# Kernel tuning notes

Hardware: AMD Instinct MI355X
Metric: run time of the kernel (lower is better)

The kernel has to match this reference:

```python
import jax, jax.numpy as jnp
import numpy as np

# Static hyperparameters (match init_kwargs)
PAD = 4          # one_side_pad_length
KL = 9           # kernel_size (= 2*PAD + 1 so L_out == output_size with stride 1)
STRIDE = 1
NLC = 8          # num_sparse_LC
OUT = 4096       # output_size


def _repeat_lengths():
    padded = OUT + 2 * PAD                      # 4104
    rough = padded // NLC                       # 513
    lens = []
    total = 0
    for i in range(NLC):
        if i == NLC - 1:
            cover = OUT - total
        else:
            cover = rough - 2 * PAD
        lens.append(cover)
        total += cover
    return lens                                  # [505]*7 + [561]


def setup_inputs() -> dict:
    key = jax.random.key(0)
    k1, k2, k3 = jax.random.split(key, 3)
    x = jax.random.normal(k1, (8, 2, 4, 64, 4096), dtype=jnp.float32)
    # weight: (dim_d, dim_k, out, in, num_sparse_LC, 1, kernel_size)
    weight = jax.random.normal(k2, (2, 4, 64, 64, 8, 1, 9), dtype=jnp.float32) * 0.05
    # conv_bias_param: (dim_d, dim_k, out, num_sparse_LC, 1)
    conv_bias_param = jax.random.normal(k3, (2, 4, 64, 8, 1), dtype=jnp.float32) * 0.02
    return {"x": x, "weight": weight, "conv_bias_param": conv_bias_param}


def reference(x, weight, conv_bias_param):
    # x: (b, d, k, in, L)
    x_pad = jnp.pad(x, ((0, 0), (0, 0), (0, 0), (0, 0), (PAD, PAD)))
    # unfold(-1, KL, 1): x_unf[..., l, f] = x_pad[..., l + f]; shape (b,d,k,in,OUT,KL)
    x_unf = jnp.stack([x_pad[..., f:f + OUT] for f in range(KL)], axis=-1)
    lens = _repeat_lengths()
    outs = []
    start = 0
    for i in range(NLC):  # small fixed loop over segments (avoids repeated-weight materialization)
        ln = lens[i]
        w = weight[:, :, :, :, i, 0, :]                 # (d, k, o, in, kl)
        xs = x_unf[:, :, :, :, start:start + ln, :]     # (b, d, k, in, ln, kl)
        o = jnp.einsum('dkoif,bdkilf->bdkol', w, xs)    # (b, d, k, o, ln)
        o = o + conv_bias_param[None, :, :, :, i, :]    # bias broadcasts over b and l
        outs.append(o)
        start += ln
    return jnp.concatenate(outs, axis=-1)               # (b, d, k, o, OUT)
```

## Files before the change

kernel.cpp:

```cpp
#include <hip/hip_runtime.h>

typedef __attribute__((ext_vector_type(8))) short bf16x8;
typedef __attribute__((ext_vector_type(4))) float f32x4;

#define WT2_BYTES (8ull * 8 * 9 * 8192)

#define AS1C(p) ((const __attribute__((address_space(1))) void*)(p))
#define AS3(p)  ((__attribute__((address_space(3))) void*)(p))

static __device__ __forceinline__ ushort f2bf(float f) {
    union { float f; unsigned u; } v; v.f = f;
    unsigned r = v.u + 0x7FFF + ((v.u >> 16) & 1);
    return (ushort)(r >> 16);
}
static __device__ __forceinline__ unsigned cvtpk(float a, float b) {
    unsigned r;
    asm("v_cvt_pk_bf16_f32 %0, %1, %2" : "=v"(r) : "v"(a), "v"(b));
    return r;
}

__global__ __launch_bounds__(256) void wprep3_kernel(const float* __restrict__ w,
                                                     ushort* __restrict__ wt) {
    __shared__ float raw[4608];
    __shared__ ushort row[72 * 64];
    int bid = blockIdx.x;
    int dk = bid >> 6, o = bid & 63;
    const float* src = w + (size_t)bid * 4608;
    int t = threadIdx.x;
    #pragma unroll
    for (int j = 0; j < 18; ++j) raw[t + 256 * j] = src[t + 256 * j];
    __syncthreads();
    int osw = o & 7;
    #pragma unroll
    for (int p = 0; p < 18; ++p) {
        int idx = t + 256 * p;
        int cf = idx >> 6, i = idx & 63;
        int c = cf / 9, f = cf - c * 9;
        row[cf * 64 + ((i >> 3) ^ osw) * 8 + (i & 7)] = f2bf(raw[i * 72 + c * 9 + f]);
    }
    __syncthreads();
    char* wb = (char*)wt + (size_t)dk * 8 * 9 * 8192 + o * 128;
    #pragma unroll
    for (int q = 0; q < 3; ++q) {
        int idx = q * 256 + t;
        if (idx < 576) {
            int cf = idx >> 3, cc = idx & 7;
            *(uint4*)(wb + (size_t)cf * 8192 + cc * 16) = *(const uint4*)&row[cf * 64 + cc * 8];
        }
    }
}

__global__ __launch_bounds__(256, 3) void conv10_kernel(
    const float* __restrict__ x, const ushort* __restrict__ wt,
    const float* __restrict__ bias, float* __restrict__ out)
{
    __shared__ __align__(16) ushort XL[136 * 64];
    __shared__ __align__(16) ushort WL[4 * 4096];

    int bid = blockIdx.x;
    int bdk = bid / 33, tile = bid - bdk * 33;
    int dk = bdk & 7;
    int c, lt;
    if (tile < 28) { c = tile >> 2; lt = tile & 3; } else { c = 7; lt = tile - 28; }
    int Sc = 505 * c, lb = lt << 7;
    int V = ((c == 7) ? 561 : 505) - lb; if (V > 128) V = 128;
    int R0 = Sc + lb;

    int t = threadIdx.x, lane = t & 63, wv = t >> 6;
    int ln16 = lane & 15, g = lane >> 4;
    int wr = wv >> 1, wc = wv & 1;
    int Lw = wr << 6, Ow = wc << 5;

    int lq = t & 31, ig = t >> 5;
    const float* xb = x + (size_t)bdk * 64 * 4096;
    float4 v[8];
    bool edge = (R0 < 4) || (R0 > 3972);
    if (!edge) {
        const float* xp = xb + (size_t)ig * 8 * 4096 + (R0 - 4 + lq * 4);
        #pragma unroll
        for (int j = 0; j < 8; ++j)
            v[j] = *(const float4*)(xp + (size_t)j * 4096);
    } else {
        #pragma unroll
        for (int j = 0; j < 8; ++j) {
            float* pv = (float*)&v[j];
            #pragma unroll
            for (int k = 0; k < 4; ++k) {
                int xr = R0 - 4 + lq * 4 + k;
                bool ok = (xr >= 0) && (xr < 4096);
                int xc = ok ? xr : 0;
                pv[k] = ok ? xb[(size_t)(ig * 8 + j) * 4096 + xc] : 0.0f;
            }
        }
    }
    float hv[8]; int rh = 0, igh = 0; bool okh = false;
    if (t < 64) {
        rh = 128 + (t >> 3);
        igh = t & 7;
        int xr = R0 - 4 + rh;
        okh = xr < 4096;
        int xc = okh ? xr : 0;
        const float* xh = xb + (size_t)igh * 8 * 4096 + xc;
        #pragma unroll
        for (int j = 0; j < 8; ++j) hv[j] = okh ? xh[(size_t)j * 4096] : 0.0f;
    }

    const char* wsl = (const char*)wt + (size_t)(dk * 8 + c) * 9 * 8192;
    auto stageW = [&](int f, int buf) {
        __builtin_amdgcn_global_load_lds(AS1C(wsl + (size_t)f * 8192 + t * 16),
                                         AS3((char*)WL + buf * 8192 + t * 16), 16, 0, 0);
        __builtin_amdgcn_global_load_lds(AS1C(wsl + (size_t)f * 8192 + 4096 + t * 16),
                                         AS3((char*)WL + buf * 8192 + 4096 + t * 16), 16, 0, 0);
    };
    stageW(0, 0); stageW(1, 1); stageW(2, 2);

    #pragma unroll
    for (int k = 0; k < 4; ++k) {
        int r = lq * 4 + k;
        uint4 A;
        A.x = cvtpk(((const float*)&v[0])[k], ((const float*)&v[1])[k]);
        A.y = cvtpk(((const float*)&v[2])[k], ((const float*)&v[3])[k]);
        A.z = cvtpk(((const float*)&v[4])[k], ((const float*)&v[5])[k]);
        A.w = cvtpk(((const float*)&v[6])[k], ((const float*)&v[7])[k]);
        *(uint4*)((char*)XL + r * 128 + ((ig ^ (r & 7)) * 16)) = A;
    }
    if (t < 64) {
        uint4 A;
        A.x = cvtpk(hv[0], hv[1]); A.y = cvtpk(hv[2], hv[3]);
        A.z = cvtpk(hv[4], hv[5]); A.w = cvtpk(hv[6], hv[7]);
        *(uint4*)((char*)XL + rh * 128 + ((igh ^ (rh & 7)) * 16)) = A;
    }

    f32x4 acc[4][2];
    #pragma unroll
    for (int a0 = 0; a0 < 4; ++a0)
        #pragma unroll
        for (int a1 = 0; a1 < 2; ++a1) acc[a0][a1] = (f32x4){0.f, 0.f, 0.f, 0.f};

    auto tap = [&](int f) {
        int buf = f & 3;
        int rbase = Lw + ln16 + f;
        int swz = rbase & 7;
        #pragma unroll
        for (int s = 0; s < 2; ++s) {
            int cof = ((s * 4 + g) ^ swz) * 16;
            int wof = buf * 8192 + ((s * 4 + g) ^ (ln16 & 7)) * 16;
            bf16x8 av[4], bv[2];
            #pragma unroll
            for (int mf = 0; mf < 4; ++mf)
                av[mf] = *(const bf16x8*)((const char*)XL + (rbase + mf * 16) * 128 + cof);
            #pragma unroll
            for (int nf = 0; nf < 2; ++nf)
                bv[nf] = *(const bf16x8*)((const char*)WL + wof + (Ow + nf * 16 + ln16) * 128);
            #pragma unroll
            for (int mf = 0; mf < 4; ++mf)
                #pragma unroll
                for (int nf = 0; nf < 2; ++nf)
                    acc[mf][nf] = __builtin_amdgcn_mfma_f32_16x16x32_bf16(av[mf], bv[nf], acc[mf][nf], 0, 0, 0);
        }
    };

    asm volatile("s_waitcnt lgkmcnt(0)" ::: "memory");

#define TAPSTEP(N, F, ISSUE) \
    asm volatile("s_waitcnt vmcnt(" #N ")" ::: "memory"); \
    __builtin_amdgcn_s_barrier(); \
    __builtin_amdgcn_sched_barrier(0); \
    if (ISSUE) stageW(F + 3, (F + 3) & 3); \
    tap(F);

    TAPSTEP(4, 0, 1) TAPSTEP(4, 1, 1) TAPSTEP(4, 2, 1) TAPSTEP(4, 3, 1)
    TAPSTEP(4, 4, 1) TAPSTEP(4, 5, 1) TAPSTEP(4, 6, 0) TAPSTEP(2, 7, 0)
    TAPSTEP(0, 8, 0)
#undef TAPSTEP

    float* ob = out + ((size_t)(bdk * 64)) * 4096 + Sc + lb;
    #pragma unroll
    for (int nf = 0; nf < 2; ++nf) {
        int o = Ow + nf * 16 + ln16;
        float bvs = bias[(dk * 64 + o) * 8 + c];
        #pragma unroll
        for (int mf = 0; mf < 4; ++mf) {
            int l = Lw + mf * 16 + g * 4;
            f32x4 vv = acc[mf][nf];
            vv[0] += bvs; vv[1] += bvs; vv[2] += bvs; vv[3] += bvs;
            if (l + 4 <= V) {
                *(f32x4*)(ob + (size_t)o * 4096 + l) = vv;
            } else if (l < V) {
                #pragma unroll
                for (int r = 0; r < 4; ++r)
                    if (l + r < V) ob[(size_t)o * 4096 + l + r] = vv[r];
            }
        }
    }
}

extern "C" void kernel_launch(void* const* d_in, const int* in_sizes, int n_in,
                              void* d_out, int out_size, void* d_ws, size_t ws_size,
                              hipStream_t stream) {
    const float* x    = (const float*)d_in[0];
    const float* wgt  = (const float*)d_in[1];
    const float* bias = (const float*)d_in[2];
    float* out        = (float*)d_out;
    ushort* wt2       = (ushort*)d_ws;

    hipLaunchKernelGGL(wprep3_kernel, dim3(512), dim3(256), 0, stream, wgt, wt2);
    hipLaunchKernelGGL(conv10_kernel, dim3(2112), dim3(256), 0, stream, x, wt2, bias, out);
}
```

Measured before the change: 55.63 us.

## Make conv kernel persistent and prefetch next tile's input during taps

Converts the one-tile-per-block conv kernel into a persistent kernel with 768 blocks striding over the 2112 tiles. The next tile's x slice is loaded into registers midway through the current tile's tap loop and written to LDS after the epilogue. This aims to hide global-load latency for x and remove per-block launch overhead and tail effects. In exchange it raises register pressure, which could hurt occupancy at 3 blocks per CU. The fixed 768-block grid may also leave an uneven tail, since 2112 tiles is not a multiple of 768.

```diff
diff --git a/kernel.cpp b/kernel.cpp
--- a/kernel.cpp
+++ b/kernel.cpp
@@ -50,93 +50,89 @@
     }
 }
 
-__global__ __launch_bounds__(256, 3) void conv10_kernel(
+__global__ __launch_bounds__(256, 3) void conv17_kernel(
     const float* __restrict__ x, const ushort* __restrict__ wt,
     const float* __restrict__ bias, float* __restrict__ out)
 {
     __shared__ __align__(16) ushort XL[136 * 64];
     __shared__ __align__(16) ushort WL[4 * 4096];
 
-    int bid = blockIdx.x;
-    int bdk = bid / 33, tile = bid - bdk * 33;
-    int dk = bdk & 7;
-    int c, lt;
-    if (tile < 28) { c = tile >> 2; lt = tile & 3; } else { c = 7; lt = tile - 28; }
-    int Sc = 505 * c, lb = lt << 7;
-    int V = ((c == 7) ? 561 : 505) - lb; if (V > 128) V = 128;
-    int R0 = Sc + lb;
-
+    const int NT = 2112, GS = 768;
     int t = threadIdx.x, lane = t & 63, wv = t >> 6;
     int ln16 = lane & 15, g = lane >> 4;
     int wr = wv >> 1, wc = wv & 1;
     int Lw = wr << 6, Ow = wc << 5;
-
     int lq = t & 31, ig = t >> 5;
-    const float* xb = x + (size_t)bdk * 64 * 4096;
-    float4 v[8];
-    bool edge = (R0 < 4) || (R0 > 3972);
-    if (!edge) {
-        const float* xp = xb + (size_t)ig * 8 * 4096 + (R0 - 4 + lq * 4);
-        #pragma unroll
-        for (int j = 0; j < 8; ++j)
-            v[j] = *(const float4*)(xp + (size_t)j * 4096);
-    } else {
-        #pragma unroll
-        for (int j = 0; j < 8; ++j) {
-            float* pv = (float*)&v[j];
-            #pragma unroll
-            for (int k = 0; k < 4; ++k) {
-                int xr = R0 - 4 + lq * 4 + k;
-                bool ok = (xr >= 0) && (xr < 4096);
-                int xc = ok ? xr : 0;
-                pv[k] = ok ? xb[(size_t)(ig * 8 + j) * 4096 + xc] : 0.0f;
+    int rh = 128 + (lane >> 3), igh = lane & 7;
+
+    auto dec = [&](int tid, int& bdk, int& dk, int& c, int& V, int& R0) {
+        bdk = tid / 33; int tile = tid - bdk * 33;
+        dk = bdk & 7;
+        int lt;
+        if (tile < 28) { c = tile >> 2; lt = tile & 3; } else { c = 7; lt = tile - 28; }
+        int lb = lt << 7;
+        V = ((c == 7) ? 561 : 505) - lb; if (V > 128) V = 128;
+        R0 = 505 * c + lb;
+    };
+
+    float4 v[8]; float hv[8];
+    auto xload = [&](int bdkX, int R0X) {
+        const float* xb = x + (size_t)bdkX * 64 * 4096;
+        bool edge = (R0X < 4) || (R0X > 3964);
+        if (!edge) {
+            const float* xp = xb + (size_t)ig * 8 * 4096 + (R0X - 4 + lq * 4);
+            #pragma unroll
+            for (int j = 0; j < 8; ++j)
+                v[j] = *(const float4*)(xp + (size_t)j * 4096);
+        } else {
+            #pragma unroll
+            for (int j = 0; j < 8; ++j) {
+                float* pv = (float*)&v[j];
+                #pragma unroll
+                for (int k = 0; k < 4; ++k) {
+                    int xr = R0X - 4 + lq * 4 + k;
+                    bool ok = (xr >= 0) && (xr < 4096);
+                    int xc = ok ? xr : 0;
+                    pv[k] = ok ? xb[(size_t)(ig * 8 + j) * 4096 + xc] : 0.0f;
+                }
             }
         }
-    }
-    float hv[8]; int rh = 0, igh = 0; bool okh = false;
-    if (t < 64) {
-        rh = 128 + (t >> 3);
-        igh = t & 7;
-        int xr = R0 - 4 + rh;
-        okh = xr < 4096;
-        int xc = okh ? xr : 0;
-        const float* xh = xb + (size_t)igh * 8 * 4096 + xc;
-        #pragma unroll
-        for (int j = 0; j < 8; ++j) hv[j] = okh ? xh[(size_t)j * 4096] : 0.0f;
-    }
-
-    const char* wsl = (const char*)wt + (size_t)(dk * 8 + c) * 9 * 8192;
-    auto stageW = [&](int f, int buf) {
+        {
+            int xr = R0X - 4 + rh;
+            bool okh = xr < 4096;
+            int xc = okh ? xr : 0;
+            const float* xh = xb + (size_t)igh * 8 * 4096 + xc;
+            #pragma unroll
+            for (int j = 0; j < 8; ++j) hv[j] = okh ? xh[(size_t)j * 4096] : 0.0f;
+        }
+    };
+    auto xwrite = [&]() {
+        #pragma unroll
+        for (int k = 0; k < 4; ++k) {
+            int r = lq * 4 + k;
+            uint4 A;
+            A.x = cvtpk(((const float*)&v[0])[k], ((const float*)&v[1])[k]);
+            A.y = cvtpk(((const float*)&v[2])[k], ((const float*)&v[3])[k]);
+            A.z = cvtpk(((const float*)&v[4])[k], ((const float*)&v[5])[k]);
+            A.w = cvtpk(((const float*)&v[6])[k], ((const float*)&v[7])[k]);
+            *(uint4*)((char*)XL + r * 128 + ((ig ^ (r & 7)) * 16)) = A;
+        }
+        {
+            uint4 A;
+            A.x = cvtpk(hv[0], hv[1]); A.y = cvtpk(hv[2], hv[3]);
+            A.z = cvtpk(hv[4], hv[5]); A.w = cvtpk(hv[6], hv[7]);
+            *(uint4*)((char*)XL + rh * 128 + ((igh ^ (rh & 7)) * 16)) = A;
+        }
+    };
+
+    auto stageW = [&](const char* wsl, int f, int buf) {
         __builtin_amdgcn_global_load_lds(AS1C(wsl + (size_t)f * 8192 + t * 16),
                                          AS3((char*)WL + buf * 8192 + t * 16), 16, 0, 0);
         __builtin_amdgcn_global_load_lds(AS1C(wsl + (size_t)f * 8192 + 4096 + t * 16),
                                          AS3((char*)WL + buf * 8192 + 4096 + t * 16), 16, 0, 0);
     };
-    stageW(0, 0); stageW(1, 1); stageW(2, 2);
-
-    #pragma unroll
-    for (int k = 0; k < 4; ++k) {
-        int r = lq * 4 + k;
-        uint4 A;
-        A.x = cvtpk(((const float*)&v[0])[k], ((const float*)&v[1])[k]);
-        A.y = cvtpk(((const float*)&v[2])[k], ((const float*)&v[3])[k]);
-        A.z = cvtpk(((const float*)&v[4])[k], ((const float*)&v[5])[k]);
-        A.w = cvtpk(((const float*)&v[6])[k], ((const float*)&v[7])[k]);
-        *(uint4*)((char*)XL + r * 128 + ((ig ^ (r & 7)) * 16)) = A;
-    }
-    if (t < 64) {
-        uint4 A;
-        A.x = cvtpk(hv[0], hv[1]); A.y = cvtpk(hv[2], hv[3]);
-        A.z = cvtpk(hv[4], hv[5]); A.w = cvtpk(hv[6], hv[7]);
-        *(uint4*)((char*)XL + rh * 128 + ((igh ^ (rh & 7)) * 16)) = A;
-    }
 
     f32x4 acc[4][2];
-    #pragma unroll
-    for (int a0 = 0; a0 < 4; ++a0)
-        #pragma unroll
-        for (int a1 = 0; a1 < 2; ++a1) acc[a0][a1] = (f32x4){0.f, 0.f, 0.f, 0.f};
-
     auto tap = [&](int f) {
         int buf = f & 3;
         int rbase = Lw + ln16 + f;
@@ -159,40 +155,81 @@
                     acc[mf][nf] = __builtin_amdgcn_mfma_f32_16x16x32_bf16(av[mf], bv[nf], acc[mf][nf], 0, 0, 0);
         }
     };
-
-    asm volatile("s_waitcnt lgkmcnt(0)" ::: "memory");
-
-#define TAPSTEP(N, F, ISSUE) \
-    asm volatile("s_waitcnt vmcnt(" #N ")" ::: "memory"); \
+    auto epilogue = [&](int bdk, int dk, int c, int V, int R0) {
+        float* ob = out + ((size_t)(bdk * 64)) * 4096 + R0;
+        #pragma unroll
+        for (int nf = 0; nf < 2; ++nf) {
+            int o = Ow + nf * 16 + ln16;
+            float bvs = bias[(dk * 64 + o) * 8 + c];
+            #pragma unroll
+            for (int mf = 0; mf < 4; ++mf) {
+                int l = Lw + mf * 16 + g * 4;
+                f32x4 vv = acc[mf][nf];
+                vv[0] += bvs; vv[1] += bvs; vv[2] += bvs; vv[3] += bvs;
+                if (l + 4 <= V) {
+                    *(f32x4*)(ob + (size_t)o * 4096 + l) = vv;
+                } else if (l < V) {
+                    #pragma unroll
+                    for (int r = 0; r < 4; ++r)
+                        if (l + r < V) ob[(size_t)o * 4096 + l + r] = vv[r];
+                }
+            }
+        }
+    };
+
+#define TS(Nstr) \
+    asm volatile("s_waitcnt vmcnt(" Nstr ") lgkmcnt(0)" ::: "memory"); \
     __builtin_amdgcn_s_barrier(); \
-    __builtin_amdgcn_sched_barrier(0); \
-    if (ISSUE) stageW(F + 3, (F + 3) & 3); \
-    tap(F);
-
-    TAPSTEP(4, 0, 1) TAPSTEP(4, 1, 1) TAPSTEP(4, 2, 1) TAPSTEP(4, 3, 1)
-    TAPSTEP(4, 4, 1) TAPSTEP(4, 5, 1) TAPSTEP(4, 6, 0) TAPSTEP(2, 7, 0)
-    TAPSTEP(0, 8, 0)
-#undef TAPSTEP
-
-    float* ob = out + ((size_t)(bdk * 64)) * 4096 + Sc + lb;
-    #pragma unroll
-    for (int nf = 0; nf < 2; ++nf) {
-        int o = Ow + nf * 16 + ln16;
-        float bvs = bias[(dk * 64 + o) * 8 + c];
-        #pragma unroll
-        for (int mf = 0; mf < 4; ++mf) {
-            int l = Lw + mf * 16 + g * 4;
-            f32x4 vv = acc[mf][nf];
-            vv[0] += bvs; vv[1] += bvs; vv[2] += bvs; vv[3] += bvs;
-            if (l + 4 <= V) {
-                *(f32x4*)(ob + (size_t)o * 4096 + l) = vv;
-            } else if (l < V) {
-                #pragma unroll
-                for (int r = 0; r < 4; ++r)
-                    if (l + r < V) ob[(size_t)o * 4096 + l + r] = vv[r];
-            }
-        }
+    __builtin_amdgcn_sched_barrier(0);
+
+    int tid = blockIdx.x;
+    int bdk, dk, c, V, R0;
+    dec(tid, bdk, dk, c, V, R0);
+    xload(bdk, R0);
+    xwrite();
+
+    while (true) {
+        const char* wsl = (const char*)wt + (size_t)(dk * 8 + c) * 9 * 8192;
+        bool pf = (tid + GS) < NT;
+        int bdkN = 0, dkN = 0, cN = 0, VN = 0, R0N = 0;
+        if (pf) dec(tid + GS, bdkN, dkN, cN, VN, R0N);
+
+        stageW(wsl, 0, 0); stageW(wsl, 1, 1); stageW(wsl, 2, 2);
+
+        #pragma unroll
+        for (int a0 = 0; a0 < 4; ++a0)
+            #pragma unroll
+            for (int a1 = 0; a1 < 2; ++a1) acc[a0][a1] = (f32x4){0.f, 0.f, 0.f, 0.f};
+
+        if (pf) {
+            TS("4")  stageW(wsl, 3, 3); tap(0);
+            TS("4")  stageW(wsl, 4, 0); tap(1);
+            TS("4")  stageW(wsl, 5, 1); tap(2);
+            TS("4")  stageW(wsl, 6, 2); tap(3);
+            TS("4")  stageW(wsl, 7, 3); tap(4);
+            TS("4")  stageW(wsl, 8, 0); xload(bdkN, R0N); tap(5);
+            TS("20") tap(6);
+            TS("18") tap(7);
+            TS("16") tap(8);
+        } else {
+            TS("4")  stageW(wsl, 3, 3); tap(0);
+            TS("4")  stageW(wsl, 4, 0); tap(1);
+            TS("4")  stageW(wsl, 5, 1); tap(2);
+            TS("4")  stageW(wsl, 6, 2); tap(3);
+            TS("4")  stageW(wsl, 7, 3); tap(4);
+            TS("4")  stageW(wsl, 8, 0); tap(5);
+            TS("4")  tap(6);
+            TS("2")  tap(7);
+            TS("0")  tap(8);
+        }
+
+        epilogue(bdk, dk, c, V, R0);
+        if (!pf) break;
+        __syncthreads();
+        xwrite();
+        tid += GS; bdk = bdkN; dk = dkN; c = cN; V = VN; R0 = R0N;
     }
+#undef TS
 }
 
 extern "C" void kernel_launch(void* const* d_in, const int* in_sizes, int n_in,
@@ -205,5 +242,5 @@
     ushort* wt2       = (ushort*)d_ws;
 
     hipLaunchKernelGGL(wprep3_kernel, dim3(512), dim3(256), 0, stream, wgt, wt2);
-    hipLaunchKernelGGL(conv10_kernel, dim3(2112), dim3(256), 0, stream, x, wt2, bias, out);
-}
+    hipLaunchKernelGGL(conv17_kernel, dim3(768), dim3(256), 0, stream, x, wt2, bias, out);
+}
```

New measurement: 57.70 us. 1.04x slower.
